# Performance work log

Hardware: AMD Instinct MI355X
Metric: run time of the kernel (lower is better)

## Reference

```python
import jax, jax.numpy as jnp
import numpy as np

D = 1024
H = 16
HD = D // H
T = 2048
B = 2
HID = 4 * D
EPS = 1e-5


def setup_inputs() -> dict:
    key = jax.random.key(0)
    ks = jax.random.split(key, 8)
    s = lambda fan_in: 1.0 / np.sqrt(fan_in)
    return {
        "x": jax.random.normal(ks[0], (B, T, D), dtype=jnp.float32),
        "ln1_g": jnp.ones((D,), jnp.float32),
        "ln1_b": jnp.zeros((D,), jnp.float32),
        "Wqkv": jax.random.uniform(ks[1], (D, 3 * D), jnp.float32, -s(D), s(D)),
        "bqkv": jnp.zeros((3 * D,), jnp.float32),
        "Wout": jax.random.uniform(ks[2], (D, D), jnp.float32, -s(D), s(D)),
        "bout": jnp.zeros((D,), jnp.float32),
        "ln2_g": jnp.ones((D,), jnp.float32),
        "ln2_b": jnp.zeros((D,), jnp.float32),
        "W1": jax.random.uniform(ks[3], (D, HID), jnp.float32, -s(D), s(D)),
        "b1": jnp.zeros((HID,), jnp.float32),
        "W2": jax.random.uniform(ks[4], (HID, D), jnp.float32, -s(HID), s(HID)),
        "b2": jnp.zeros((D,), jnp.float32),
    }


def _layernorm(h, g, b):
    mu = jnp.mean(h, axis=-1, keepdims=True)
    var = jnp.mean(jnp.square(h - mu), axis=-1, keepdims=True)
    return (h - mu) * jax.lax.rsqrt(var + EPS) * g + b


def reference(x, ln1_g, ln1_b, Wqkv, bqkv, Wout, bout, ln2_g, ln2_b, W1, b1, W2, b2):
    b, t, d = x.shape
    scale = 1.0 / np.sqrt(HD)

    # --- attention (pre-LN) ---
    h = _layernorm(x, ln1_g, ln1_b)
    qkv = h @ Wqkv + bqkv                      # [b, t, 3d]
    q, k, v = jnp.split(qkv, 3, axis=-1)
    q = q.reshape(b, t, H, HD)
    k = k.reshape(b, t, H, HD)
    v = v.reshape(b, t, H, HD)
    scores = jnp.einsum("bqhd,bkhd->bhqk", q, k) * scale  # [b, h, t, t]
    causal = jnp.tril(jnp.ones((t, t), dtype=bool))
    scores = jnp.where(causal, scores, -jnp.inf)
    attn = jax.nn.softmax(scores, axis=-1)
    out = jnp.einsum("bhqk,bkhd->bqhd", attn, v).reshape(b, t, d)
    x = x + (out @ Wout + bout)

    # --- MLP (pre-LN) ---
    h = _layernorm(x, ln2_g, ln2_b)
    h = jax.nn.gelu(h @ W1 + b1, approximate=False)
    x = x + (h @ W2 + b2)
    return x
```

## Files before the change

kernel.cpp:

```cpp
#include <hip/hip_runtime.h>
#include <hip/hip_bf16.h>
#include <math.h>

#define DD 1024
#define TT 2048
#define BB 2
#define HH 16
#define HDIM 64
#define HIDD 4096

typedef __attribute__((ext_vector_type(4))) float f32x4;
typedef __attribute__((ext_vector_type(8))) __bf16 bf16x8;
typedef __attribute__((ext_vector_type(4))) __bf16 bf16x4;

#define MF16 __builtin_amdgcn_mfma_f32_16x16x32_bf16

__device__ __forceinline__ void gload_lds16(const void* g, void* l) {
  __builtin_amdgcn_global_load_lds(
      (const __attribute__((address_space(1))) void*)g,
      (__attribute__((address_space(3))) void*)l, 16, 0, 0);
}

__global__ __launch_bounds__(256) void castT64(const float* __restrict__ W,
                                               __bf16* __restrict__ Wt,
                                               int K, int N) {
  __shared__ float t[64][65];
  const int n0 = blockIdx.x * 64, k0 = blockIdx.y * 64;
#pragma unroll
  for (int e = 0; e < 16; ++e) {
    int idx = e * 256 + threadIdx.x;
    int rr = idx >> 6, cc = idx & 63;
    t[rr][cc] = W[(size_t)(k0 + rr) * N + n0 + cc];
  }
  __syncthreads();
#pragma unroll
  for (int e = 0; e < 16; ++e) {
    int idx = e * 256 + threadIdx.x;
    int rr = idx >> 6, cc = idx & 63;
    Wt[(size_t)(n0 + rr) * K + k0 + cc] = (__bf16)t[cc][rr];
  }
}

__global__ __launch_bounds__(256) void ln_fwd(const float* __restrict__ x,
                                              const float* __restrict__ gamma,
                                              const float* __restrict__ beta,
                                              __bf16* __restrict__ out) {
  const int row = blockIdx.x;
  const int t4 = threadIdx.x;
  const float4 v = reinterpret_cast<const float4*>(x + (size_t)row * DD)[t4];
  float s = v.x + v.y + v.z + v.w;
  float ss = v.x * v.x + v.y * v.y + v.z * v.z + v.w * v.w;
#pragma unroll
  for (int m = 32; m >= 1; m >>= 1) { s += __shfl_xor(s, m); ss += __shfl_xor(ss, m); }
  __shared__ float red[8];
  const int wave = threadIdx.x >> 6, lane = threadIdx.x & 63;
  if (lane == 0) { red[wave] = s; red[4 + wave] = ss; }
  __syncthreads();
  s = red[0] + red[1] + red[2] + red[3];
  ss = red[4] + red[5] + red[6] + red[7];
  const float mu = s * (1.0f / DD);
  const float rs = rsqrtf(ss * (1.0f / DD) - mu * mu + 1e-5f);
  const float4 gm = reinterpret_cast<const float4*>(gamma)[t4];
  const float4 bt = reinterpret_cast<const float4*>(beta)[t4];
  bf16x4 o;
  o[0] = (__bf16)((v.x - mu) * rs * gm.x + bt.x);
  o[1] = (__bf16)((v.y - mu) * rs * gm.y + bt.y);
  o[2] = (__bf16)((v.z - mu) * rs * gm.z + bt.z);
  o[3] = (__bf16)((v.w - mu) * rs * gm.w + bt.w);
  *reinterpret_cast<bf16x4*>(out + (size_t)row * DD + t4 * 4) = o;
}

template <int MODE>
__global__ __launch_bounds__(512, 1) void gemm8(const __bf16* __restrict__ A,
                                                const __bf16* __restrict__ Bt,
                                                const float* __restrict__ bias,
                                                const float* __restrict__ resid,
                                                void* __restrict__ out0,
                                                void* __restrict__ q1,
                                                void* __restrict__ q2,
                                                void* __restrict__ q3,
                                                int N, int K, int kchunk) {
  const int tid = threadIdx.x;
  const int wid = tid >> 6, lane = tid & 63;
  const int g = lane >> 4, r = lane & 15;
  const int wrh = wid >> 2;
  const int wc = (wid & 3) * 64;

  const int gx = gridDim.x, gy = gridDim.y;
  const int nwg = gx * gy;
  const int orig = blockIdx.y * gx + blockIdx.x;
  const int swz = (orig & 7) * (nwg >> 3) + (orig >> 3);
  const int bn4 = swz & 3;
  const int bmt = (swz >> 2) % gx;
  const int bng = (swz >> 2) / gx;
  const int bm = bmt * 256;
  const int bn = (bng * 4 + bn4) * 256;

  const int kbase = blockIdx.z * kchunk;
  const int NT = kchunk >> 6;
  const __bf16* Asrc = A + (size_t)bm * K + kbase;
  const __bf16* Bsrc = Bt + (size_t)bn * K + kbase;

  __shared__ __bf16 lds[2][4][8192];

  f32x4 acc[8][4] = {};
  bf16x8 bfr[4][2];

  auto STG = [&](int ab, int h, int kt) {
    const __bf16* src = (ab ? Bsrc : Asrc) + (size_t)h * 128 * K;
    char* dst = (char*)&lds[kt & 1][ab * 2 + h][0];
#pragma unroll
    for (int gl = 0; gl < 2; ++gl) {
      const int o = gl * 8192 + wid * 1024 + lane * 16;
      const int row = o >> 7;
      const int cbs = (o & 127) ^ (((row >> 2) & 1) << 5);
      gload_lds16((const char*)src + (size_t)row * (K * 2) + kt * 128 + cbs,
                  dst + gl * 8192 + wid * 1024);
    }
  };
  auto DSA = [&](int s, int mi, int kk) -> bf16x8 {
    return *(const bf16x8*)((const char*)&lds[s][wrh][0] + (mi * 16 + r) * 128 +
                            ((kk * 64 + g * 16) ^ ((r & 4) << 3)));
  };
  auto DSB = [&](int s, int nj, int kk) -> bf16x8 {
    const int rt = wc + nj * 16 + r;
    return *(const bf16x8*)((const char*)&lds[s][2 + (rt >> 7)][0] + (rt & 127) * 128 +
                            ((kk * 64 + g * 16) ^ ((r & 4) << 3)));
  };

#define PH(S, Q, STAGE_STMT, WAIT_STMT)                                        \
  {                                                                            \
    if (Q == 0) {                                                              \
      _Pragma("unroll") for (int nj = 0; nj < 4; ++nj) {                       \
        bfr[nj][0] = DSB(S, nj, 0);                                            \
        bfr[nj][1] = DSB(S, nj, 1);                                            \
      }                                                                        \
    }                                                                          \
    bf16x8 a00 = DSA(S, 2 * Q, 0), a01 = DSA(S, 2 * Q, 1);                     \
    bf16x8 a10 = DSA(S, 2 * Q + 1, 0), a11 = DSA(S, 2 * Q + 1, 1);             \
    STAGE_STMT;                                                                \
    WAIT_STMT;                                                                 \
    __builtin_amdgcn_s_barrier();                                              \
    asm volatile("s_waitcnt lgkmcnt(0)" ::: "memory");                         \
    __builtin_amdgcn_s_setprio(1);                                             \
    _Pragma("unroll") for (int nj = 0; nj < 4; ++nj) {                         \
      acc[2 * Q][nj] = MF16(a00, bfr[nj][0], acc[2 * Q][nj], 0, 0, 0);         \
      acc[2 * Q][nj] = MF16(a01, bfr[nj][1], acc[2 * Q][nj], 0, 0, 0);         \
      acc[2 * Q + 1][nj] = MF16(a10, bfr[nj][0], acc[2 * Q + 1][nj], 0, 0, 0); \
      acc[2 * Q + 1][nj] = MF16(a11, bfr[nj][1], acc[2 * Q + 1][nj], 0, 0, 0); \
    }                                                                          \
    __builtin_amdgcn_s_setprio(0);                                             \
    __builtin_amdgcn_s_barrier();                                              \
  }

  STG(1, 0, 0); STG(1, 1, 0); STG(0, 0, 0); STG(0, 1, 0);
  STG(1, 0, 1); STG(1, 1, 1); STG(0, 0, 1);
  asm volatile("s_waitcnt vmcnt(6)" ::: "memory");
  __builtin_amdgcn_s_barrier();

  const int NI = NT >> 1;
  for (int i = 0; i < NI; ++i) {
    const int k2 = 2 * i + 2, k3 = 2 * i + 3;
    const bool nl = (i + 1 < NI);
    PH(0, 0, { STG(0, 1, 2 * i + 1); }, {});
    PH(0, 1, { if (nl) STG(1, 0, k2); }, {});
    PH(0, 2, { if (nl) STG(1, 1, k2); }, {});
    PH(0, 3, { if (nl) STG(0, 0, k2); },
       { if (nl) asm volatile("s_waitcnt vmcnt(6)" ::: "memory");
         else    asm volatile("s_waitcnt vmcnt(0)" ::: "memory"); });
    PH(1, 0, { if (nl) STG(0, 1, k2); }, {});
    PH(1, 1, { if (nl) STG(1, 0, k3); }, {});
    PH(1, 2, { if (nl) STG(1, 1, k3); }, {});
    PH(1, 3, { if (nl) STG(0, 0, k3); },
       { if (nl) asm volatile("s_waitcnt vmcnt(6)" ::: "memory"); });
  }
#undef PH

  const int row0 = bm + wrh * 128 + g * 4;
  const int col0 = bn + wc + r;
#pragma unroll
  for (int mi = 0; mi < 8; ++mi) {
#pragma unroll
    for (int nj = 0; nj < 4; ++nj) {
      const int col = col0 + nj * 16;
      const float bv = bias[col];
#pragma unroll
      for (int i4 = 0; i4 < 4; ++i4) {
        const int rowg = row0 + mi * 16 + i4;
        const size_t idx = (size_t)rowg * N + col;
        const float v = acc[mi][nj][i4];
        if (MODE == 0) {
          ((__bf16*)out0)[idx] = (__bf16)(v + bv);
        } else if (MODE == 2) {
          const float t = v + bv;
          const float u2 = t * (1.5957691216f + t * t * 0.0713548163f);
          ((__bf16*)out0)[idx] = (__bf16)(t * __builtin_amdgcn_rcpf(1.0f + __expf(-u2)));
        } else {
          if (blockIdx.z == 0) {
            ((float*)out0)[idx] = v + bv + resid[idx];
          } else {
            __bf16* p = (__bf16*)(blockIdx.z == 1 ? q1 : (blockIdx.z == 2 ? q2 : q3));
            p[idx] = (__bf16)v;
          }
        }
      }
    }
  }
}

__global__ __launch_bounds__(256) void reduceW2(const __bf16* __restrict__ p1,
                                                const __bf16* __restrict__ p2,
                                                const __bf16* __restrict__ p3,
                                                float* __restrict__ out) {
  const size_t i8 = ((size_t)blockIdx.x * 256 + threadIdx.x) * 8;
  bf16x8 a = *(const bf16x8*)(p1 + i8);
  bf16x8 b = *(const bf16x8*)(p2 + i8);
  bf16x8 c = *(const bf16x8*)(p3 + i8);
  float4 o0 = *(float4*)(out + i8);
  float4 o1 = *(float4*)(out + i8 + 4);
  float* op0 = (float*)&o0;
  float* op1 = (float*)&o1;
#pragma unroll
  for (int j = 0; j < 4; ++j) op0[j] += (float)a[j] + (float)b[j] + (float)c[j];
#pragma unroll
  for (int j = 0; j < 4; ++j) op1[j] += (float)a[4 + j] + (float)b[4 + j] + (float)c[4 + j];
  *(float4*)(out + i8) = o0;
  *(float4*)(out + i8 + 4) = o1;
}

template <int MODE>
__global__ __launch_bounds__(256) void gemm_bt(const __bf16* __restrict__ A,
                                               const __bf16* __restrict__ Bt,
                                               const float* __restrict__ bias,
                                               const float* __restrict__ resid,
                                               void* __restrict__ Cout,
                                               int M, int N, int K) {
  __shared__ __bf16 As[128 * 32];
  __shared__ __bf16 Bs[128 * 32];
  const int tid = threadIdx.x;
  const int wave = tid >> 6, lane = tid & 63;
  const int g = lane >> 4, r = lane & 15;
  const int gx = gridDim.x;
  const int nwg = gx * gridDim.y;
  const int orig = blockIdx.y * gx + blockIdx.x;
  const int swz = (orig & 7) * (nwg >> 3) + (orig >> 3);
  const int bn4 = swz & 3;
  const int bmt = (swz >> 2) % gx;
  const int bng = (swz >> 2) / gx;
  const int bm = bmt * 128;
  const int bn = (bng * 4 + bn4) * 128;
  const int wr = (wave >> 1) * 64, wc = (wave & 1) * 64;
  f32x4 acc[4][4] = {};

  const int off0 = wave * 2048 + lane * 16;
  const int off1 = off0 + 1024;
  const int sr0 = off0 >> 6, sk0 = (off0 & 63) >> 1;
  const int sr1 = off1 >> 6, sk1 = (off1 & 63) >> 1;
  const __bf16* gA0 = A + (size_t)(bm + sr0) * K + sk0;
  const __bf16* gA1 = A + (size_t)(bm + sr1) * K + sk1;
  const __bf16* gB0 = Bt + (size_t)(bn + sr0) * K + sk0;
  const __bf16* gB1 = Bt + (size_t)(bn + sr1) * K + sk1;
  char* lA0 = (char*)As + wave * 2048;
  char* lA1 = lA0 + 1024;
  char* lB0 = (char*)Bs + wave * 2048;
  char* lB1 = lB0 + 1024;

  for (int k0 = 0; k0 < K; k0 += 32) {
    gload_lds16(gA0 + k0, lA0);
    gload_lds16(gA1 + k0, lA1);
    gload_lds16(gB0 + k0, lB0);
    gload_lds16(gB1 + k0, lB1);
    __syncthreads();
    bf16x8 af[4], bf[4];
#pragma unroll
    for (int mi = 0; mi < 4; ++mi)
      af[mi] = *reinterpret_cast<const bf16x8*>(&As[(wr + mi * 16 + r) * 32 + g * 8]);
#pragma unroll
    for (int ni = 0; ni < 4; ++ni)
      bf[ni] = *reinterpret_cast<const bf16x8*>(&Bs[(wc + ni * 16 + r) * 32 + g * 8]);
    __builtin_amdgcn_s_setprio(1);
#pragma unroll
    for (int mi = 0; mi < 4; ++mi)
#pragma unroll
      for (int ni = 0; ni < 4; ++ni)
        acc[mi][ni] = MF16(af[mi], bf[ni], acc[mi][ni], 0, 0, 0);
    __builtin_amdgcn_s_setprio(0);
    __syncthreads();
  }

  const int row0 = bm + wr + 4 * g;
  const int col0 = bn + wc + r;
#pragma unroll
  for (int mi = 0; mi < 4; ++mi) {
#pragma unroll
    for (int ni = 0; ni < 4; ++ni) {
      const int col = col0 + ni * 16;
      const float bv = bias[col];
#pragma unroll
      for (int i = 0; i < 4; ++i) {
        const int row = row0 + mi * 16 + i;
        const size_t idx = (size_t)row * N + col;
        float v = acc[mi][ni][i] + bv;
        if (MODE == 0) {
          ((__bf16*)Cout)[idx] = (__bf16)v;
        } else if (MODE == 1) {
          ((float*)Cout)[idx] = v + resid[idx];
        } else {
          const float u2 = v * (1.5957691216f + v * v * 0.0713548163f);
          const float gl = v * __builtin_amdgcn_rcpf(1.0f + __expf(-u2));
          ((__bf16*)Cout)[idx] = (__bf16)gl;
        }
      }
    }
  }
}

__global__ __launch_bounds__(256) void vtrans(const __bf16* __restrict__ qkv,
                                              __bf16* __restrict__ vtg) {
  const int bh = blockIdx.y, b = bh >> 4, h = bh & 15;
  const int t0 = blockIdx.x * 64;
  const int tid = threadIdx.x, wave = tid >> 6, lane = tid & 63;
  __shared__ __bf16 tile[64 * 64];
#pragma unroll
  for (int e = 0; e < 2; ++e) {
    const int gid = e * 256 + tid;
    const int row = gid >> 3, d0 = (gid & 7) * 8;
    bf16x8 v = *reinterpret_cast<const bf16x8*>(
        qkv + (size_t)(b * TT + t0 + row) * 3072 + 2048 + h * 64 + d0);
    const int slot = (d0 >> 3) ^ (row & 7);
    *reinterpret_cast<bf16x8*>((char*)tile + row * 128 + slot * 16) = v;
  }
  __syncthreads();
  const int d = lane;
#pragma unroll
  for (int e = 0; e < 2; ++e) {
    const int k0 = (wave * 2 + e) * 8;
    bf16x8 o;
#pragma unroll
    for (int j = 0; j < 8; ++j) {
      const int row = k0 + j;
      o[j] = *(const __bf16*)((const char*)tile + row * 128 +
                              (((d >> 3) ^ (row & 7)) << 4) + (d & 7) * 2);
    }
    *reinterpret_cast<bf16x8*>(&vtg[((size_t)bh * 64 + d) * 2048 + t0 + k0]) = o;
  }
}

__device__ __forceinline__ void stage_kv(const __bf16* __restrict__ src_row0, int rstride,
                                         int wave, int lane, char* tile) {
#pragma unroll
  for (int qq = 0; qq < 2; ++qq) {
    const int o = wave * 2048 + qq * 1024 + lane * 16;
    const int p = o >> 12, row = (o >> 6) & 63, cb = (o >> 4) & 3;
    gload_lds16(src_row0 + (size_t)row * rstride + p * 32 + cb * 8,
                tile + wave * 2048 + qq * 1024);
  }
}

__global__ __launch_bounds__(256) void attn_fwd(const __bf16* __restrict__ qkv,
                                                const __bf16* __restrict__ vtg,
                                                __bf16* __restrict__ atto) {
  const int orig = blockIdx.y * gridDim.x + blockIdx.x;
  const int swz = (orig & 7) * 64 + (orig >> 3);
  const int bh = swz >> 4;
  const int j = swz & 15;
  const int b = bh >> 4, h = bh & 15;
  const int tid = threadIdx.x;
  const int wave = tid >> 6, lane = tid & 63;
  const int g = lane >> 4, r = lane & 15;

  __shared__ __bf16 Qs[2 * 64 * 32];
  __shared__ __bf16 Ks[2][2 * 64 * 32];
  __shared__ __bf16 Vs[2][2 * 64 * 32];
  __shared__ __bf16 Pl[4][2 * 16 * 32];

  const __bf16* ksrc = qkv + (size_t)(b * TT) * 3072 + 1024 + h * 64;
  const __bf16* vsrc = vtg + (size_t)bh * 64 * 2048;
  const float C2 = 0.18033688011112042f;

  for (int ph = 0; ph < 2; ++ph) {
    const int qt = ph ? (31 - j) : j;
    const int q0 = qt * 64;
    stage_kv(qkv + (size_t)(b * TT + q0) * 3072 + h * 64, 3072, wave, lane, (char*)Qs);
    stage_kv(ksrc, 3072, wave, lane, (char*)Ks[0]);
    stage_kv(vsrc, 2048, wave, lane, (char*)Vs[0]);

    f32x4 oacc[4] = {};
    float m_s[4], l_s[4];
#pragma unroll
    for (int i = 0; i < 4; ++i) { m_s[i] = -1e30f; l_s[i] = 0.0f; }

    const int nt = qt + 1;
    int cur = 0;
    for (int t = 0; t < nt; ++t) {
      const int kv0 = t * 64;
      __syncthreads();
      if (t + 1 < nt) {
        stage_kv(ksrc + (size_t)(kv0 + 64) * 3072, 3072, wave, lane, (char*)Ks[cur ^ 1]);
        stage_kv(vsrc + kv0 + 64, 2048, wave, lane, (char*)Vs[cur ^ 1]);
      }
      bf16x8 qf[2];
#pragma unroll
      for (int kp = 0; kp < 2; ++kp)
        qf[kp] = *reinterpret_cast<const bf16x8*>(&Qs[kp * 2048 + (wave * 16 + r) * 32 + g * 8]);
      f32x4 s[4];
#pragma unroll
      for (int cn = 0; cn < 4; ++cn) s[cn] = f32x4{0.f, 0.f, 0.f, 0.f};
      __builtin_amdgcn_s_setprio(1);
#pragma unroll
      for (int cn = 0; cn < 4; ++cn)
#pragma unroll
        for (int kp = 0; kp < 2; ++kp) {
          bf16x8 bk = *reinterpret_cast<const bf16x8*>(
              &Ks[cur][kp * 2048 + (cn * 16 + r) * 32 + g * 8]);
          s[cn] = MF16(qf[kp], bk, s[cn], 0, 0, 0);
        }
      __builtin_amdgcn_s_setprio(0);
      const int rowg = q0 + wave * 16 + 4 * g;
      float pm[4];
#pragma unroll
      for (int i = 0; i < 4; ++i) pm[i] = -1e30f;
#pragma unroll
      for (int cn = 0; cn < 4; ++cn) {
        const int colg = kv0 + cn * 16 + r;
#pragma unroll
        for (int i = 0; i < 4; ++i) {
          float v = s[cn][i] * C2;
          v = (colg > rowg + i) ? -1e30f : v;
          s[cn][i] = v;
          pm[i] = fmaxf(pm[i], v);
        }
      }
      const int upd = __any((pm[0] > m_s[0] + 8.0f) || (pm[1] > m_s[1] + 8.0f) ||
                            (pm[2] > m_s[2] + 8.0f) || (pm[3] > m_s[3] + 8.0f));
      if (upd) {
#pragma unroll
        for (int i = 0; i < 4; ++i) {
          pm[i] = fmaxf(pm[i], __shfl_xor(pm[i], 1));
          pm[i] = fmaxf(pm[i], __shfl_xor(pm[i], 2));
          pm[i] = fmaxf(pm[i], __shfl_xor(pm[i], 4));
          pm[i] = fmaxf(pm[i], __shfl_xor(pm[i], 8));
          const float mn = fmaxf(m_s[i], pm[i]);
          const float sf = __builtin_amdgcn_exp2f(m_s[i] - mn);
          m_s[i] = mn;
          l_s[i] *= sf;
#pragma unroll
          for (int ni = 0; ni < 4; ++ni) oacc[ni][i] *= sf;
        }
      }
      float psum[4] = {0.f, 0.f, 0.f, 0.f};
#pragma unroll
      for (int cn = 0; cn < 4; ++cn)
#pragma unroll
        for (int i = 0; i < 4; ++i) {
          const float p = __builtin_amdgcn_exp2f(s[cn][i] - m_s[i]);
          s[cn][i] = p;
          psum[i] += p;
        }
#pragma unroll
      for (int i = 0; i < 4; ++i) {
        psum[i] += __shfl_xor(psum[i], 1);
        psum[i] += __shfl_xor(psum[i], 2);
        psum[i] += __shfl_xor(psum[i], 4);
        psum[i] += __shfl_xor(psum[i], 8);
        l_s[i] += psum[i];
      }
#pragma unroll
      for (int cn = 0; cn < 4; ++cn)
#pragma unroll
        for (int i = 0; i < 4; ++i)
          Pl[wave][(cn >> 1) * 512 + (4 * g + i) * 32 + (cn & 1) * 16 + r] = (__bf16)s[cn][i];
      bf16x8 pa[2];
#pragma unroll
      for (int kp = 0; kp < 2; ++kp)
        pa[kp] = *reinterpret_cast<const bf16x8*>(&Pl[wave][kp * 512 + r * 32 + g * 8]);
      __builtin_amdgcn_s_setprio(1);
#pragma unroll
      for (int ni = 0; ni < 4; ++ni)
#pragma unroll
        for (int kp = 0; kp < 2; ++kp) {
          bf16x8 bv = *reinterpret_cast<const bf16x8*>(
              &Vs[cur][kp * 2048 + (ni * 16 + r) * 32 + g * 8]);
          oacc[ni] = MF16(pa[kp], bv, oacc[ni], 0, 0, 0);
        }
      __builtin_amdgcn_s_setprio(0);
      cur ^= 1;
    }

#pragma unroll
    for (int i = 0; i < 4; ++i) {
      const float inv = 1.0f / l_s[i];
      const size_t rowo = (size_t)(b * TT + q0 + wave * 16 + 4 * g + i) * DD + h * 64;
#pragma unroll
      for (int ni = 0; ni < 4; ++ni)
        atto[rowo + ni * 16 + r] = (__bf16)(oacc[ni][i] * inv);
    }
    __syncthreads();
  }
}

extern "C" void kernel_launch(void* const* d_in, const int* in_sizes, int n_in,
                              void* d_out, int out_size, void* d_ws, size_t ws_size,
                              hipStream_t stream) {
  const float* x     = (const float*)d_in[0];
  const float* ln1_g = (const float*)d_in[1];
  const float* ln1_b = (const float*)d_in[2];
  const float* Wqkv  = (const float*)d_in[3];
  const float* bqkv  = (const float*)d_in[4];
  const float* Wout  = (const float*)d_in[5];
  const float* bout  = (const float*)d_in[6];
  const float* ln2_g = (const float*)d_in[7];
  const float* ln2_b = (const float*)d_in[8];
  const float* W1    = (const float*)d_in[9];
  const float* b1    = (const float*)d_in[10];
  const float* W2    = (const float*)d_in[11];
  const float* b2    = (const float*)d_in[12];
  float* out = (float*)d_out;

  char* ws = (char*)d_ws;
  const size_t MB = 1024 * 1024;
  __bf16* WqkvT = (__bf16*)(ws);
  __bf16* WoutT = (__bf16*)(ws + 6 * MB);
  __bf16* W1T   = (__bf16*)(ws + 8 * MB);
  __bf16* W2T   = (__bf16*)(ws + 16 * MB);
  float*  x1    = (float*)(ws + 24 * MB);
  __bf16* hbuf  = (__bf16*)(ws + 40 * MB);
  __bf16* vtg   = (__bf16*)(ws + 40 * MB);
  __bf16* qkvb  = (__bf16*)(ws + 48 * MB);
  __bf16* atto  = (__bf16*)(ws + 72 * MB);
  __bf16* mlp1  = (__bf16*)(ws + 48 * MB);
  __bf16* p1b   = (__bf16*)(ws);
  __bf16* p2b   = (__bf16*)(ws + 8 * MB);
  __bf16* p3b   = (__bf16*)(ws + 40 * MB);

  castT64<<<dim3(48, 16), 256, 0, stream>>>(Wqkv, WqkvT, 1024, 3072);
  castT64<<<dim3(16, 16), 256, 0, stream>>>(Wout, WoutT, 1024, 1024);
  castT64<<<dim3(64, 16), 256, 0, stream>>>(W1, W1T, 1024, 4096);
  castT64<<<dim3(16, 64), 256, 0, stream>>>(W2, W2T, 4096, 1024);

  ln_fwd<<<4096, 256, 0, stream>>>(x, ln1_g, ln1_b, hbuf);
  gemm8<0><<<dim3(16, 12), 512, 0, stream>>>(hbuf, WqkvT, bqkv, nullptr, qkvb,
                                             nullptr, nullptr, nullptr, 3072, 1024, 1024);
  vtrans<<<dim3(32, 32), 256, 0, stream>>>(qkvb, vtg);
  attn_fwd<<<dim3(16, 32), 256, 0, stream>>>(qkvb, vtg, atto);
  gemm_bt<1><<<dim3(32, 8), 256, 0, stream>>>(atto, WoutT, bout, x, x1, 4096, 1024, 1024);

  ln_fwd<<<4096, 256, 0, stream>>>(x1, ln2_g, ln2_b, hbuf);
  gemm8<2><<<dim3(16, 16), 512, 0, stream>>>(hbuf, W1T, b1, nullptr, mlp1,
                                             nullptr, nullptr, nullptr, 4096, 1024, 1024);
  gemm8<3><<<dim3(16, 4, 4), 512, 0, stream>>>(mlp1, W2T, b2, x1, out,
                                               p1b, p2b, p3b, 1024, 4096, 1024);
  reduceW2<<<2048, 256, 0, stream>>>(p1b, p2b, p3b, out);
}
```

Baseline: 279.7 us.

## Fuse V transpose into QKV GEMM and split-K W2 via atomics

The QKV GEMM epilogue now writes the V part directly in transposed [b,h,d,t] layout, which removes the separate vtrans kernel. The W2 split-K GEMM now atomically adds fp32 partials into the output, and the second layernorm pre-initialises that output with x1+b2. This drops the bf16 partial buffers and the reduceW2 kernel. In exchange, the transposed V stores are strided and uncoalesced, there is atomic traffic on 4x the output, and the summation order becomes nondeterministic.

```diff
diff --git a/kernel.cpp b/kernel.cpp
--- a/kernel.cpp
+++ b/kernel.cpp
@@ -41,10 +41,13 @@
   }
 }
 
+template <int PRE>
 __global__ __launch_bounds__(256) void ln_fwd(const float* __restrict__ x,
                                               const float* __restrict__ gamma,
                                               const float* __restrict__ beta,
-                                              __bf16* __restrict__ out) {
+                                              __bf16* __restrict__ out,
+                                              const float* __restrict__ pb,
+                                              float* __restrict__ outp) {
   const int row = blockIdx.x;
   const int t4 = threadIdx.x;
   const float4 v = reinterpret_cast<const float4*>(x + (size_t)row * DD)[t4];
@@ -68,17 +71,20 @@
   o[2] = (__bf16)((v.z - mu) * rs * gm.z + bt.z);
   o[3] = (__bf16)((v.w - mu) * rs * gm.w + bt.w);
   *reinterpret_cast<bf16x4*>(out + (size_t)row * DD + t4 * 4) = o;
+  if (PRE) {
+    const float4 bb = reinterpret_cast<const float4*>(pb)[t4];
+    float4 p;
+    p.x = v.x + bb.x; p.y = v.y + bb.y; p.z = v.z + bb.z; p.w = v.w + bb.w;
+    reinterpret_cast<float4*>(outp + (size_t)row * DD)[t4] = p;
+  }
 }
 
 template <int MODE>
 __global__ __launch_bounds__(512, 1) void gemm8(const __bf16* __restrict__ A,
                                                 const __bf16* __restrict__ Bt,
                                                 const float* __restrict__ bias,
-                                                const float* __restrict__ resid,
                                                 void* __restrict__ out0,
-                                                void* __restrict__ q1,
-                                                void* __restrict__ q2,
-                                                void* __restrict__ q3,
+                                                __bf16* __restrict__ q1,
                                                 int N, int K, int kchunk) {
   const int tid = threadIdx.x;
   const int wid = tid >> 6, lane = tid & 63;
@@ -86,17 +92,27 @@
   const int wrh = wid >> 2;
   const int wc = (wid & 3) * 64;
 
-  const int gx = gridDim.x, gy = gridDim.y;
-  const int nwg = gx * gy;
-  const int orig = blockIdx.y * gx + blockIdx.x;
-  const int swz = (orig & 7) * (nwg >> 3) + (orig >> 3);
-  const int bn4 = swz & 3;
-  const int bmt = (swz >> 2) % gx;
-  const int bng = (swz >> 2) / gx;
-  const int bm = bmt * 256;
-  const int bn = (bng * 4 + bn4) * 256;
-
-  const int kbase = blockIdx.z * kchunk;
+  int bm, bn, kbase;
+  if constexpr (MODE == 3) {
+    const int L = blockIdx.x;
+    const int xcd = L & 7, idx = L >> 3;
+    const int z = xcd >> 1;
+    bm = (((xcd & 1) << 3) + (idx >> 2)) * 256;
+    bn = (idx & 3) * 256;
+    kbase = z * kchunk;
+  } else {
+    const int gx = gridDim.x;
+    const int nwg = gx * gridDim.y;
+    const int orig = blockIdx.y * gx + blockIdx.x;
+    const int swz = (orig & 7) * (nwg >> 3) + (orig >> 3);
+    const int bn4 = swz & 3;
+    const int bmt = (swz >> 2) % gx;
+    const int bng = (swz >> 2) / gx;
+    bm = bmt * 256;
+    bn = (bng * 4 + bn4) * 256;
+    kbase = 0;
+  }
+
   const int NT = kchunk >> 6;
   const __bf16* Asrc = A + (size_t)bm * K + kbase;
   const __bf16* Bsrc = Bt + (size_t)bn * K + kbase;
@@ -183,49 +199,32 @@
 #pragma unroll
     for (int nj = 0; nj < 4; ++nj) {
       const int col = col0 + nj * 16;
-      const float bv = bias[col];
+      float bv = 0.0f;
+      if constexpr (MODE != 3) bv = bias[col];
 #pragma unroll
       for (int i4 = 0; i4 < 4; ++i4) {
         const int rowg = row0 + mi * 16 + i4;
         const size_t idx = (size_t)rowg * N + col;
         const float v = acc[mi][nj][i4];
-        if (MODE == 0) {
-          ((__bf16*)out0)[idx] = (__bf16)(v + bv);
-        } else if (MODE == 2) {
+        if constexpr (MODE == 0) {
+          if (bn >= 2048) {
+            const int cv = col - 2048;
+            const int hv = cv >> 6, dv = cv & 63;
+            const int bq = rowg >> 11, tq = rowg & 2047;
+            q1[(((size_t)bq * 16 + hv) * 64 + dv) * 2048 + tq] = (__bf16)(v + bv);
+          } else {
+            ((__bf16*)out0)[idx] = (__bf16)(v + bv);
+          }
+        } else if constexpr (MODE == 2) {
           const float t = v + bv;
           const float u2 = t * (1.5957691216f + t * t * 0.0713548163f);
           ((__bf16*)out0)[idx] = (__bf16)(t * __builtin_amdgcn_rcpf(1.0f + __expf(-u2)));
         } else {
-          if (blockIdx.z == 0) {
-            ((float*)out0)[idx] = v + bv + resid[idx];
-          } else {
-            __bf16* p = (__bf16*)(blockIdx.z == 1 ? q1 : (blockIdx.z == 2 ? q2 : q3));
-            p[idx] = (__bf16)v;
-          }
+          atomicAdd((float*)out0 + idx, v);
         }
       }
     }
   }
-}
-
-__global__ __launch_bounds__(256) void reduceW2(const __bf16* __restrict__ p1,
-                                                const __bf16* __restrict__ p2,
-                                                const __bf16* __restrict__ p3,
-                                                float* __restrict__ out) {
-  const size_t i8 = ((size_t)blockIdx.x * 256 + threadIdx.x) * 8;
-  bf16x8 a = *(const bf16x8*)(p1 + i8);
-  bf16x8 b = *(const bf16x8*)(p2 + i8);
-  bf16x8 c = *(const bf16x8*)(p3 + i8);
-  float4 o0 = *(float4*)(out + i8);
-  float4 o1 = *(float4*)(out + i8 + 4);
-  float* op0 = (float*)&o0;
-  float* op1 = (float*)&o1;
-#pragma unroll
-  for (int j = 0; j < 4; ++j) op0[j] += (float)a[j] + (float)b[j] + (float)c[j];
-#pragma unroll
-  for (int j = 0; j < 4; ++j) op1[j] += (float)a[4 + j] + (float)b[4 + j] + (float)c[4 + j];
-  *(float4*)(out + i8) = o0;
-  *(float4*)(out + i8 + 4) = o1;
 }
 
 template <int MODE>
@@ -315,37 +314,6 @@
   }
 }
 
-__global__ __launch_bounds__(256) void vtrans(const __bf16* __restrict__ qkv,
-                                              __bf16* __restrict__ vtg) {
-  const int bh = blockIdx.y, b = bh >> 4, h = bh & 15;
-  const int t0 = blockIdx.x * 64;
-  const int tid = threadIdx.x, wave = tid >> 6, lane = tid & 63;
-  __shared__ __bf16 tile[64 * 64];
-#pragma unroll
-  for (int e = 0; e < 2; ++e) {
-    const int gid = e * 256 + tid;
-    const int row = gid >> 3, d0 = (gid & 7) * 8;
-    bf16x8 v = *reinterpret_cast<const bf16x8*>(
-        qkv + (size_t)(b * TT + t0 + row) * 3072 + 2048 + h * 64 + d0);
-    const int slot = (d0 >> 3) ^ (row & 7);
-    *reinterpret_cast<bf16x8*>((char*)tile + row * 128 + slot * 16) = v;
-  }
-  __syncthreads();
-  const int d = lane;
-#pragma unroll
-  for (int e = 0; e < 2; ++e) {
-    const int k0 = (wave * 2 + e) * 8;
-    bf16x8 o;
-#pragma unroll
-    for (int j = 0; j < 8; ++j) {
-      const int row = k0 + j;
-      o[j] = *(const __bf16*)((const char*)tile + row * 128 +
-                              (((d >> 3) ^ (row & 7)) << 4) + (d & 7) * 2);
-    }
-    *reinterpret_cast<bf16x8*>(&vtg[((size_t)bh * 64 + d) * 2048 + t0 + k0]) = o;
-  }
-}
-
 __device__ __forceinline__ void stage_kv(const __bf16* __restrict__ src_row0, int rstride,
                                          int wave, int lane, char* tile) {
 #pragma unroll
@@ -524,31 +492,23 @@
   __bf16* W1T   = (__bf16*)(ws + 8 * MB);
   __bf16* W2T   = (__bf16*)(ws + 16 * MB);
   float*  x1    = (float*)(ws + 24 * MB);
+  __bf16* vtg   = (__bf16*)(ws + 24 * MB);
   __bf16* hbuf  = (__bf16*)(ws + 40 * MB);
-  __bf16* vtg   = (__bf16*)(ws + 40 * MB);
   __bf16* qkvb  = (__bf16*)(ws + 48 * MB);
   __bf16* atto  = (__bf16*)(ws + 72 * MB);
   __bf16* mlp1  = (__bf16*)(ws + 48 * MB);
-  __bf16* p1b   = (__bf16*)(ws);
-  __bf16* p2b   = (__bf16*)(ws + 8 * MB);
-  __bf16* p3b   = (__bf16*)(ws + 40 * MB);
 
   castT64<<<dim3(48, 16), 256, 0, stream>>>(Wqkv, WqkvT, 1024, 3072);
   castT64<<<dim3(16, 16), 256, 0, stream>>>(Wout, WoutT, 1024, 1024);
   castT64<<<dim3(64, 16), 256, 0, stream>>>(W1, W1T, 1024, 4096);
   castT64<<<dim3(16, 64), 256, 0, stream>>>(W2, W2T, 4096, 1024);
 
-  ln_fwd<<<4096, 256, 0, stream>>>(x, ln1_g, ln1_b, hbuf);
-  gemm8<0><<<dim3(16, 12), 512, 0, stream>>>(hbuf, WqkvT, bqkv, nullptr, qkvb,
-                                             nullptr, nullptr, nullptr, 3072, 1024, 1024);
-  vtrans<<<dim3(32, 32), 256, 0, stream>>>(qkvb, vtg);
+  ln_fwd<0><<<4096, 256, 0, stream>>>(x, ln1_g, ln1_b, hbuf, nullptr, nullptr);
+  gemm8<0><<<dim3(16, 12), 512, 0, stream>>>(hbuf, WqkvT, bqkv, qkvb, vtg, 3072, 1024, 1024);
   attn_fwd<<<dim3(16, 32), 256, 0, stream>>>(qkvb, vtg, atto);
   gemm_bt<1><<<dim3(32, 8), 256, 0, stream>>>(atto, WoutT, bout, x, x1, 4096, 1024, 1024);
 
-  ln_fwd<<<4096, 256, 0, stream>>>(x1, ln2_g, ln2_b, hbuf);
-  gemm8<2><<<dim3(16, 16), 512, 0, stream>>>(hbuf, W1T, b1, nullptr, mlp1,
-                                             nullptr, nullptr, nullptr, 4096, 1024, 1024);
-  gemm8<3><<<dim3(16, 4, 4), 512, 0, stream>>>(mlp1, W2T, b2, x1, out,
-                                               p1b, p2b, p3b, 1024, 4096, 1024);
-  reduceW2<<<2048, 256, 0, stream>>>(p1b, p2b, p3b, out);
-}
+  ln_fwd<1><<<4096, 256, 0, stream>>>(x1, ln2_g, ln2_b, hbuf, b2, out);
+  gemm8<2><<<dim3(16, 16), 512, 0, stream>>>(hbuf, W1T, b1, mlp1, nullptr, 4096, 1024, 1024);
+  gemm8<3><<<dim3(256, 1), 512, 0, stream>>>(mlp1, W2T, b2, out, nullptr, 1024, 4096, 1024);
+}
```

Measured after the change: 298.4 us. +6.7%, slower.
